# Kernel optimization log

Hardware: AMD Instinct MI355X
Metric: run time of the kernel (lower is better)

The kernel has to match this reference:

```python
import jax, jax.numpy as jnp
from jax import lax
import numpy as np

NODE = 100000
D = 256      # input_dim
H = 256      # hidden_dim
P = 4096     # num paths between the pair
L = 8        # path length (hops)
OUT = 1


def setup_inputs() -> dict:
    key = jax.random.key(0)
    ks = jax.random.split(key, 10)
    s = 1.0 / np.sqrt(H)
    return {
        "embedding": jax.random.normal(ks[0], (NODE, D), jnp.float32) * 0.1,
        "w_ih": jax.random.normal(ks[1], (4 * H, D), jnp.float32) * s,
        "w_hh": jax.random.normal(ks[2], (4 * H, H), jnp.float32) * s,
        "b_ih": jax.random.normal(ks[3], (4 * H,), jnp.float32) * s,
        "b_hh": jax.random.normal(ks[4], (4 * H,), jnp.float32) * s,
        "w_lin": jax.random.normal(ks[5], (OUT, H + 2 * D), jnp.float32) * 0.05,
        "b_lin": jax.random.normal(ks[6], (OUT,), jnp.float32) * 0.05,
        "paths": jax.random.randint(ks[7], (P, L), 0, NODE, jnp.int64),
        "user_id": jax.random.randint(ks[8], (1,), 0, NODE, jnp.int64),
        "item_id": jax.random.randint(ks[9], (1,), 0, NODE, jnp.int64),
    }


def _lstm_final_hidden(x, w_ih, w_hh, b_ih, b_hh):
    # x: [P, L, D] -> final hidden state h_n: [P, H] (PyTorch gate order i,f,g,o)
    p, _, _ = x.shape
    h = x.shape  # noqa (shape comment)
    hidden = w_hh.shape[1]
    b = b_ih + b_hh

    def step(carry, x_t):
        h, c = carry
        gates = x_t @ w_ih.T + h @ w_hh.T + b  # [P, 4H]
        i, f, g, o = jnp.split(gates, 4, axis=-1)
        c = jax.nn.sigmoid(f) * c + jax.nn.sigmoid(i) * jnp.tanh(g)
        h = jax.nn.sigmoid(o) * jnp.tanh(c)
        return (h, c), None

    h0 = jnp.zeros((p, hidden), x.dtype)
    c0 = jnp.zeros((p, hidden), x.dtype)
    (h_n, _), _ = lax.scan(step, (h0, c0), jnp.swapaxes(x, 0, 1))  # scan over L
    return h_n


def reference(embedding, w_ih, w_hh, b_ih, b_hh, w_lin, b_lin, paths, user_id, item_id):
    # Batched version of the per-path loop: embed all paths, one LSTM scan.
    x = embedding[paths]                                   # [P, L, D]
    sum_hidden = _lstm_final_hidden(x, w_ih, w_hh, b_ih, b_hh)  # [P, H] (== stacked h_n)

    # MaxPool2d((1, H)) over hidden dim -> attention logits over paths
    att = jnp.max(sum_hidden, axis=-1, keepdims=True)      # [P, 1]
    att = jax.nn.softmax(att, axis=0)                      # softmax over paths
    path_emb = jnp.sum(sum_hidden * att, axis=0, keepdims=True)  # [1, H]

    user_emb = embedding[user_id]                          # [1, D]
    item_emb = embedding[item_id]                          # [1, D]
    emb = jnp.concatenate([user_emb, item_emb, path_emb], axis=-1)  # [1, 2D+H]
    out = jax.nn.sigmoid(emb @ w_lin.T + b_lin)            # [1, OUT]
    return out
```

## Files before the change

kernel.cpp:

```cpp
#include <hip/hip_runtime.h>
#include <stdint.h>

#define NPATHS 4096
#define LPATH  8
#define DIM    256
#define HID    256

typedef short  short4v __attribute__((ext_vector_type(4)));
typedef short  short8v __attribute__((ext_vector_type(8)));
typedef float  float4v __attribute__((ext_vector_type(4)));

__device__ __forceinline__ unsigned short f2bf(float f) {
    union { float f; uint32_t u; } v; v.f = f;
    uint32_t u = v.u;
    u += 0x7FFFu + ((u >> 16) & 1u);
    return (unsigned short)(u >> 16);
}
__device__ __forceinline__ float bf2f(unsigned short s) {
    return __uint_as_float(((uint32_t)s) << 16);
}
__device__ __forceinline__ float fast_sigmoid(float x) {
    return 1.0f / (1.0f + __expf(-x));
}
__device__ __forceinline__ float fast_tanh(float x) {
    x = fminf(15.0f, fmaxf(-15.0f, x));
    float e = __expf(2.0f * x);
    return (e - 1.0f) / (e + 1.0f);
}

__global__ void prep_kernel(const float* __restrict__ w_ih, const float* __restrict__ w_hh,
                            const float* __restrict__ b_ih, const float* __restrict__ b_hh,
                            unsigned short* __restrict__ WfB, float* __restrict__ bias,
                            float* __restrict__ path_emb, unsigned int* __restrict__ done) {
    int gid  = blockIdx.x * 256 + threadIdx.x;
    int base = gid * 4;
    int j0   = base & 7;
    int unit = (base >> 3) & 255;
    int quad = (base >> 11) & 3;
    int gkc  = base >> 13;
    int g    = gkc >> 4, kc = gkc & 15;
    int row  = g * 256 + unit;
    int k    = kc * 32 + quad * 8 + j0;
    const float* src = (k < DIM) ? (w_ih + (size_t)row * DIM + k)
                                 : (w_hh + (size_t)row * HID + (k - DIM));
    float4 v = *(const float4*)src;
    short4v pk = {(short)f2bf(v.x), (short)f2bf(v.y), (short)f2bf(v.z), (short)f2bf(v.w)};
    *(short4v*)(WfB + base) = pk;
    if (gid < 1024) bias[gid] = b_ih[gid] + b_hh[gid];
    if (gid < 256)  path_emb[gid] = 0.0f;
    if (gid == 0)   *done = 0u;
}

__global__ __launch_bounds__(1024)
__attribute__((amdgpu_waves_per_eu(4, 4)))
void mega_kernel(const float* __restrict__ embedding, const int* __restrict__ paths,
                 const unsigned short* __restrict__ WfB, const float* __restrict__ bias,
                 unsigned short* __restrict__ h_final, float* __restrict__ logits) {
    __shared__ __align__(16) short sAx[8 * 512];
    __shared__ __align__(16) short h_lds[16 * 256];
    __shared__ float red[16 * 16];

    const int tid  = threadIdx.x;
    const int w    = tid >> 6;
    const int lane = tid & 63;
    const int l15  = lane & 15;
    const int quad = lane >> 4;
    const int p0   = blockIdx.x * 16;
    const int unit = w * 16 + l15;

    const short* bb0 = (const short*)WfB + quad * 2048 + unit * 8;

    float bb[4];
#pragma unroll
    for (int g = 0; g < 4; ++g) bb[g] = bias[g * 256 + unit];

    const int grow = tid & 15;
    const int gk0  = (tid >> 4) * 4;
    const int gdst = (gk0 >> 5) * 512 + (((gk0 >> 3) & 3) * 16 + grow) * 8 + (gk0 & 4);
    {
        int node = paths[(p0 + grow) * LPATH];
        float4v v = __builtin_nontemporal_load(
            (const float4v*)(embedding + (size_t)node * DIM + gk0));
        short4v pk = {(short)f2bf(v[0]), (short)f2bf(v[1]),
                      (short)f2bf(v[2]), (short)f2bf(v[3])};
        *(short4v*)(&sAx[gdst]) = pk;
    }

    float cc[4] = {0.0f, 0.0f, 0.0f, 0.0f};

    __syncthreads();

#pragma unroll 1
    for (int t = 0; t < LPATH; ++t) {
        const bool first = (t == 0), last = (t == LPATH - 1);
        const int  K     = first ? 8 : 16;

        float4v gv;
        if (!last) {
            int node = paths[(p0 + grow) * LPATH + t + 1];
            gv = __builtin_nontemporal_load(
                (const float4v*)(embedding + (size_t)node * DIM + gk0));
        }

        float4v acc[4];
        const float4v z4 = {0.0f, 0.0f, 0.0f, 0.0f};
#pragma unroll
        for (int g = 0; g < 4; ++g) acc[g] = z4;

#pragma unroll 1
        for (int kc = 0; kc < K; ++kc) {
            short8v a;
            if (kc < 8) {
                a = *(const short8v*)(sAx + kc * 512 + lane * 8);
            } else {
                int cg  = (kc - 8) * 4 + quad;
                int cgs = cg ^ (l15 & 7);
                a = *(const short8v*)(&h_lds[l15 * 256 + cgs * 8]);
            }
            const short* bk = bb0 + kc * 8192;
            short8v bf0 = *(const short8v*)(bk);
            short8v bf1 = *(const short8v*)(bk + 131072);
            short8v bf2 = *(const short8v*)(bk + 262144);
            short8v bf3 = *(const short8v*)(bk + 393216);
            acc[0] = __builtin_amdgcn_mfma_f32_16x16x32_bf16(a, bf0, acc[0], 0, 0, 0);
            acc[1] = __builtin_amdgcn_mfma_f32_16x16x32_bf16(a, bf1, acc[1], 0, 0, 0);
            acc[2] = __builtin_amdgcn_mfma_f32_16x16x32_bf16(a, bf2, acc[2], 0, 0, 0);
            acc[3] = __builtin_amdgcn_mfma_f32_16x16x32_bf16(a, bf3, acc[3], 0, 0, 0);
        }

        __syncthreads();

        if (!last) {
            short4v pk = {(short)f2bf(gv[0]), (short)f2bf(gv[1]),
                          (short)f2bf(gv[2]), (short)f2bf(gv[3])};
            *(short4v*)(&sAx[gdst]) = pk;
        }

        float hv[4];
#pragma unroll
        for (int r = 0; r < 4; ++r) {
            float iv = acc[0][r] + bb[0];
            float fv = acc[1][r] + bb[1];
            float gg = acc[2][r] + bb[2];
            float ov = acc[3][r] + bb[3];
            float cn = fast_sigmoid(fv) * cc[r] + fast_sigmoid(iv) * fast_tanh(gg);
            cc[r] = cn;
            hv[r] = fast_sigmoid(ov) * fast_tanh(cn);
        }

#pragma unroll
        for (int r = 0; r < 4; ++r) {
            int pr  = quad * 4 + r;
            int cgs = (unit >> 3) ^ (pr & 7);
            h_lds[pr * 256 + cgs * 8 + (unit & 7)] = (short)f2bf(hv[r]);
        }

        if (last) {
#pragma unroll
            for (int r = 0; r < 4; ++r) {
                float m = hv[r];
                m = fmaxf(m, __shfl_xor(m, 1, 64));
                m = fmaxf(m, __shfl_xor(m, 2, 64));
                m = fmaxf(m, __shfl_xor(m, 4, 64));
                m = fmaxf(m, __shfl_xor(m, 8, 64));
                if (l15 == 0) red[(quad * 4 + r) * 16 + w] = m;
            }
        }
        __syncthreads();
    }

    if (tid < 16) {
        float m = red[tid * 16];
#pragma unroll
        for (int j = 1; j < 16; ++j) m = fmaxf(m, red[tid * 16 + j]);
        logits[p0 + tid] = m;
    }
    if (tid < 512) {
        int row = tid >> 5, i5 = tid & 31;
        int cgs = i5 ^ (row & 7);
        short8v v = *(const short8v*)(&h_lds[row * 256 + cgs * 8]);
        *(short8v*)(h_final + (size_t)(p0 + row) * HID + (size_t)i5 * 8) = v;
    }
}

__global__ void attn_final_kernel(const unsigned short* __restrict__ h_final,
                                  const float* __restrict__ logits,
                                  float* __restrict__ path_emb,
                                  unsigned int* __restrict__ done,
                                  const float* __restrict__ embedding,
                                  const int* __restrict__ user_id,
                                  const int* __restrict__ item_id,
                                  const float* __restrict__ w_lin,
                                  const float* __restrict__ b_lin,
                                  float* __restrict__ out) {
    __shared__ float red[256];
    __shared__ float wts[16];
    __shared__ int lastf;
    int tid = threadIdx.x;
    int p0  = blockIdx.x * 16;

    float vals[16];
    float m = -1e30f;
#pragma unroll
    for (int i = 0; i < 16; ++i) {
        vals[i] = logits[i * 256 + tid];
        m = fmaxf(m, vals[i]);
    }
    red[tid] = m; __syncthreads();
    for (int s = 128; s > 0; s >>= 1) {
        if (tid < s) red[tid] = fmaxf(red[tid], red[tid + s]);
        __syncthreads();
    }
    m = red[0]; __syncthreads();
    float sum = 0.0f;
#pragma unroll
    for (int i = 0; i < 16; ++i) sum += __expf(vals[i] - m);
    red[tid] = sum; __syncthreads();
    for (int s = 128; s > 0; s >>= 1) {
        if (tid < s) red[tid] += red[tid + s];
        __syncthreads();
    }
    if (tid == 0) red[0] = 1.0f / red[0];
    __syncthreads();
    float invZ = red[0];
    if (tid < 16) wts[tid] = __expf(logits[p0 + tid] - m) * invZ;
    __syncthreads();

    float acc = 0.0f;
#pragma unroll
    for (int j = 0; j < 16; ++j)
        acc += wts[j] * bf2f(h_final[(size_t)(p0 + j) * HID + tid]);
    atomicAdd(&path_emb[tid], acc);

    __threadfence();
    __syncthreads();
    if (tid == 0) {
        unsigned int old = atomicAdd(done, 1u);
        lastf = (old == 255u) ? 1 : 0;
    }
    __syncthreads();
    if (lastf) {
        __threadfence();
        float pe = __hip_atomic_load(&path_emb[tid], __ATOMIC_RELAXED,
                                     __HIP_MEMORY_SCOPE_AGENT);
        int u  = user_id[0];
        int it = item_id[0];
        float s = w_lin[tid]       * embedding[(size_t)u  * DIM + tid]
                + w_lin[256 + tid] * embedding[(size_t)it * DIM + tid]
                + w_lin[512 + tid] * pe;
        red[tid] = s; __syncthreads();
        for (int st = 128; st > 0; st >>= 1) {
            if (tid < st) red[tid] += red[tid + st];
            __syncthreads();
        }
        if (tid == 0) out[0] = 1.0f / (1.0f + __expf(-(red[0] + b_lin[0])));
    }
}

extern "C" void kernel_launch(void* const* d_in, const int* in_sizes, int n_in,
                              void* d_out, int out_size, void* d_ws, size_t ws_size,
                              hipStream_t stream) {
    const float* embedding = (const float*)d_in[0];
    const float* w_ih      = (const float*)d_in[1];
    const float* w_hh      = (const float*)d_in[2];
    const float* b_ih      = (const float*)d_in[3];
    const float* b_hh      = (const float*)d_in[4];
    const float* w_lin     = (const float*)d_in[5];
    const float* b_lin     = (const float*)d_in[6];
    const int*   paths     = (const int*)d_in[7];
    const int*   user_id   = (const int*)d_in[8];
    const int*   item_id   = (const int*)d_in[9];
    float* outp = (float*)d_out;

    char* ws = (char*)d_ws;
    size_t off = 0;
    auto alloc = [&](size_t n) { void* p = ws + off; off = (off + n + 255) & ~(size_t)255; return p; };
    unsigned short* WfB      = (unsigned short*)alloc((size_t)1024 * 512 * 2);
    float*          bias     = (float*)alloc(1024 * 4);
    float*          path_emb = (float*)alloc(HID * 4);
    float*          logits   = (float*)alloc(NPATHS * 4);
    unsigned short* h_final  = (unsigned short*)alloc((size_t)NPATHS * HID * 2);
    unsigned int*   done     = (unsigned int*)alloc(4);

    prep_kernel<<<512, 256, 0, stream>>>(w_ih, w_hh, b_ih, b_hh, WfB, bias,
                                         path_emb, done);

    mega_kernel<<<256, 1024, 0, stream>>>(embedding, paths, WfB, bias,
                                          h_final, logits);

    attn_final_kernel<<<256, 256, 0, stream>>>(h_final, logits, path_emb, done,
                                               embedding, user_id, item_id,
                                               w_lin, b_lin, outp);
}
```

Measured before the change: 259.2 us.

## Software-pipeline weight and activation loads in MFMA loop with per-block K rotation

Restructures the inner K loop so that the weight fragments and A operand for the next iteration are loaded while the current MFMAs issue, hiding global/L2 and LDS latency. It also rotates the starting K chunk by block index so that concurrent blocks hit different weight rows, spreading cache/channel traffic. The last prefetch wraps around to the next timestep's first chunk, which adds register pressure under the fixed waves-per-EU bound.

After: 257.0 us. Within noise of the previous version (-0.9%).

```diff
diff --git a/kernel.cpp b/kernel.cpp
--- a/kernel.cpp
+++ b/kernel.cpp
@@ -67,6 +67,7 @@
     const int quad = lane >> 4;
     const int p0   = blockIdx.x * 16;
     const int unit = w * 16 + l15;
+    const int roff = blockIdx.x & 7;
 
     const short* bb0 = (const short*)WfB + quad * 2048 + unit * 8;
 
@@ -90,10 +91,19 @@
 
     __syncthreads();
 
+    short8v pf0, pf1, pf2, pf3;
+    {
+        const short* bk = bb0 + roff * 8192;
+        pf0 = *(const short8v*)(bk);
+        pf1 = *(const short8v*)(bk + 131072);
+        pf2 = *(const short8v*)(bk + 262144);
+        pf3 = *(const short8v*)(bk + 393216);
+    }
+
 #pragma unroll 1
     for (int t = 0; t < LPATH; ++t) {
-        const bool first = (t == 0), last = (t == LPATH - 1);
-        const int  K     = first ? 8 : 16;
+        const bool last = (t == LPATH - 1);
+        const int  K    = (t == 0) ? 8 : 16;
 
         float4v gv;
         if (!last) {
@@ -107,25 +117,32 @@
 #pragma unroll
         for (int g = 0; g < 4; ++g) acc[g] = z4;
 
+        short8v pa = *(const short8v*)(sAx + roff * 512 + lane * 8);
+
 #pragma unroll 1
-        for (int kc = 0; kc < K; ++kc) {
-            short8v a;
-            if (kc < 8) {
-                a = *(const short8v*)(sAx + kc * 512 + lane * 8);
+        for (int i = 0; i < K; ++i) {
+            int ip  = i + 1;
+            int kcn = (ip < K) ? ((ip < 8) ? ((ip + roff) & 7)
+                                           : (8 + ((ip + roff) & 7)))
+                               : roff;
+            const short* bk = bb0 + kcn * 8192;
+
+            acc[0] = __builtin_amdgcn_mfma_f32_16x16x32_bf16(pa, pf0, acc[0], 0, 0, 0);
+            pf0 = *(const short8v*)(bk);
+            acc[1] = __builtin_amdgcn_mfma_f32_16x16x32_bf16(pa, pf1, acc[1], 0, 0, 0);
+            pf1 = *(const short8v*)(bk + 131072);
+            acc[2] = __builtin_amdgcn_mfma_f32_16x16x32_bf16(pa, pf2, acc[2], 0, 0, 0);
+            pf2 = *(const short8v*)(bk + 262144);
+            acc[3] = __builtin_amdgcn_mfma_f32_16x16x32_bf16(pa, pf3, acc[3], 0, 0, 0);
+            pf3 = *(const short8v*)(bk + 393216);
+
+            if (kcn < 8) {
+                pa = *(const short8v*)(sAx + kcn * 512 + lane * 8);
             } else {
-                int cg  = (kc - 8) * 4 + quad;
+                int cg  = (kcn - 8) * 4 + quad;
                 int cgs = cg ^ (l15 & 7);
-                a = *(const short8v*)(&h_lds[l15 * 256 + cgs * 8]);
+                pa = *(const short8v*)(&h_lds[l15 * 256 + cgs * 8]);
             }
-            const short* bk = bb0 + kc * 8192;
-            short8v bf0 = *(const short8v*)(bk);
-            short8v bf1 = *(const short8v*)(bk + 131072);
-            short8v bf2 = *(const short8v*)(bk + 262144);
-            short8v bf3 = *(const short8v*)(bk + 393216);
-            acc[0] = __builtin_amdgcn_mfma_f32_16x16x32_bf16(a, bf0, acc[0], 0, 0, 0);
-            acc[1] = __builtin_amdgcn_mfma_f32_16x16x32_bf16(a, bf1, acc[1], 0, 0, 0);
-            acc[2] = __builtin_amdgcn_mfma_f32_16x16x32_bf16(a, bf2, acc[2], 0, 0, 0);
-            acc[3] = __builtin_amdgcn_mfma_f32_16x16x32_bf16(a, bf3, acc[3], 0, 0, 0);
         }
 
         __syncthreads();
```
